# Kernel optimization log

Measured on AMD Instinct MI355X. Metric: run time of the kernel, lower is better.

The kernel has to match this reference:

```python
import jax, jax.numpy as jnp
from jax import lax
import numpy as np

B, S, V, E, H = 256, 1024, 288, 100, 128


def setup_inputs() -> dict:
    key = jax.random.key(0)
    ks = jax.random.split(key, 16)
    d = {
        "text": jax.random.randint(ks[0], (B, S), 0, V, dtype=jnp.int32),
        "emb": jax.random.normal(ks[1], (V, E), jnp.float32) * 0.1,
        "fcW": jax.random.normal(ks[2], (V, H), jnp.float32) * 0.1,
        "fcb": jax.random.normal(ks[3], (V,), jnp.float32) * 0.1,
    }
    in_dims = [E, H, H]
    for l in range(3):
        kk = jax.random.split(ks[4 + l], 4)
        d[f"Wih{l}"] = jax.random.normal(kk[0], (4 * H, in_dims[l]), jnp.float32) * 0.1
        d[f"Whh{l}"] = jax.random.normal(kk[1], (4 * H, H), jnp.float32) * 0.1
        d[f"bih{l}"] = jax.random.normal(kk[2], (4 * H,), jnp.float32) * 0.1
        d[f"bhh{l}"] = jax.random.normal(kk[3], (4 * H,), jnp.float32) * 0.1
    return d


def _lstm_layer(x, Wih, Whh, bih, bhh):
    # x: [S, B, in]; PyTorch gate order i, f, g, o
    xg = jnp.einsum('sbe,ge->sbg', x, Wih) + (bih + bhh)  # precompute input proj [S,B,4H]
    Hh = Whh.shape[1]
    WhhT = Whh.T

    def step(carry, xg_t):
        h, c = carry
        g = xg_t + h @ WhhT
        i, f, gg, o = jnp.split(g, 4, axis=-1)
        c = jax.nn.sigmoid(f) * c + jax.nn.sigmoid(i) * jnp.tanh(gg)
        h = jax.nn.sigmoid(o) * jnp.tanh(c)
        return (h, c), h

    b = x.shape[1]
    init = (jnp.zeros((b, Hh), x.dtype), jnp.zeros((b, Hh), x.dtype))
    _, hs = lax.scan(step, init, xg)
    return hs  # [S, B, H]


def reference(text, emb, Wih0, Whh0, bih0, bhh0, Wih1, Whh1, bih1, bhh1,
              Wih2, Whh2, bih2, bhh2, fcW, fcb):
    # embedding (dropout is identity in eval mode)
    x = emb[text]                  # [B, S, E]
    x = jnp.transpose(x, (1, 0, 2))  # time-major [S, B, E]
    x = _lstm_layer(x, Wih0, Whh0, bih0, bhh0)
    x = _lstm_layer(x, Wih1, Whh1, bih1, bhh1)
    x = _lstm_layer(x, Wih2, Whh2, bih2, bhh2)
    # fc head; original returns prediction.transpose(0,1) -> [S, B, V]
    pred = jnp.einsum('sbh,vh->sbv', x, fcW) + fcb
    return pred
```

## Files before the change

### kernel.cpp

```cpp
#include <hip/hip_runtime.h>
#include <cstddef>
#include <cstdint>

#define BB 256
#define SS 1024
#define VV 288
#define EE 100
#define HH 128
#define G4 512
#define CH 16
#define NCH (SS / CH)

typedef _Float16 half8 __attribute__((ext_vector_type(8)));
typedef float f32x4 __attribute__((ext_vector_type(4)));
typedef float f32x2 __attribute__((ext_vector_type(2)));

__device__ __forceinline__ f32x2 exp2_2(f32x2 a) {
    f32x2 r;
    r[0] = __builtin_amdgcn_exp2f(a[0]);
    r[1] = __builtin_amdgcn_exp2f(a[1]);
    return r;
}
__device__ __forceinline__ f32x2 rcp_2(f32x2 a) {
    f32x2 r;
    r[0] = __builtin_amdgcn_rcpf(a[0]);
    r[1] = __builtin_amdgcn_rcpf(a[1]);
    return r;
}
__device__ __forceinline__ f32x2 vmin2(f32x2 a, float m) {
    f32x2 r;
    r[0] = fminf(a[0], m);
    r[1] = fminf(a[1], m);
    return r;
}

__device__ __forceinline__ f32x2 lstm_pair(
    f32x2 gi, f32x2 gf, f32x2 gg, f32x2 go, f32x2& cc)
{
    const float L1 = -1.4426950408889634f;
    const float L2 = -2.8853900817779268f;
    const f32x2 one = {1.0f, 1.0f};
    f32x2 ai = exp2_2(gi * L1);
    f32x2 bg = exp2_2(vmin2(gg * L2, 80.0f));
    f32x2 af = exp2_2(gf * L1);
    f32x2 sf = rcp_2(af + one);
    f32x2 it = (one - bg) * rcp_2((ai + one) * (bg + one));
    cc = __builtin_elementwise_fma(sf, cc, it);
    f32x2 dc = exp2_2(vmin2(cc * L2, 80.0f));
    f32x2 ao = exp2_2(go * L1);
    return (one - dc) * rcp_2((ao + one) * (dc + one));
}

__global__ __launch_bounds__(512) void proj_kernel(
    const float* __restrict__ emb, const float* __restrict__ Wih0,
    const float* __restrict__ bih0, const float* __restrict__ bhh0,
    float* __restrict__ table)
{
    __shared__ float er[EE];
    const int v = blockIdx.x;
    const int j = threadIdx.x;
    for (int e = j; e < EE; e += 512) er[e] = emb[v * EE + e];
    __syncthreads();
    float acc = bih0[j] + bhh0[j];
    const float* wr = Wih0 + j * EE;
#pragma unroll 4
    for (int e = 0; e < EE; e++) acc = fmaf(er[e], wr[e], acc);
    table[v * G4 + j] = acc;
}

__global__ __launch_bounds__(256) void pack_fc(
    const float* __restrict__ W, _Float16* __restrict__ out)
{
    const int tid = blockIdx.x * 256 + threadIdx.x;
    const int e  = tid & 7;
    const int l  = (tid >> 3) & 63;
    const int f  = tid >> 9;
    const int kc = f & 3, nt = f >> 2;
    const int n = nt * 16 + (l & 15);
    const int k = kc * 32 + (l >> 4) * 8 + e;
    out[tid] = (_Float16)W[n * HH + k];
}

__global__ __launch_bounds__(512)
__attribute__((amdgpu_waves_per_eu(2, 2)))
void lstm_pipe(const int* __restrict__ text, const float* __restrict__ table,
               const float* Whh0f,
               const float* Wih1f, const float* Whh1f,
               const float* __restrict__ bih1, const float* __restrict__ bhh1,
               const float* Wih2f, const float* Whh2f,
               const float* __restrict__ bih2, const float* __restrict__ bhh2,
               _Float16* hX, _Float16* hY, int* prog)
{
    __shared__ int tokL[SS * 16];
    __shared__ _Float16 Hb[2][2048];
    const int tid = threadIdx.x;
    const int w = tid >> 6, l = tid & 63;
    const int layer = blockIdx.x >> 4;
    const int bt = blockIdx.x & 15;
    const int B0 = bt * 16;
    const int colD = l & 15, qd = l >> 4;
    const int gcol = w * 16 + colD;

    const float* WhhF = (layer == 0) ? Whh0f : ((layer == 1) ? Whh1f : Whh2f);
    const float* WihF = (layer == 2) ? Wih2f : Wih1f;
    const float* bihp = (layer == 2) ? bih2 : bih1;
    const float* bhhp = (layer == 2) ? bhh2 : bhh1;
    const _Float16* xin = (layer == 1) ? hX : hY;
    _Float16* hout = (layer == 1) ? hY : hX;
    int* prog_src = prog + (layer - 1) * 16 + bt;
    int* prog_my  = prog + layer * 16 + bt;

    half8 whh[4][4], wih[4][4];
#pragma unroll
    for (int gt = 0; gt < 4; gt++)
#pragma unroll
        for (int kc = 0; kc < 4; kc++) {
            const int n = gt * 128 + gcol;
            const int k0 = kc * 32 + qd * 8;
            const float4 a0 = *(const float4*)(WhhF + (size_t)n * HH + k0);
            const float4 a1 = *(const float4*)(WhhF + (size_t)n * HH + k0 + 4);
            half8 hf;
            hf[0] = (_Float16)a0.x; hf[1] = (_Float16)a0.y;
            hf[2] = (_Float16)a0.z; hf[3] = (_Float16)a0.w;
            hf[4] = (_Float16)a1.x; hf[5] = (_Float16)a1.y;
            hf[6] = (_Float16)a1.z; hf[7] = (_Float16)a1.w;
            whh[gt][kc] = hf;
            if (layer) {
                const float4 b0 = *(const float4*)(WihF + (size_t)n * HH + k0);
                const float4 b1 = *(const float4*)(WihF + (size_t)n * HH + k0 + 4);
                half8 hg;
                hg[0] = (_Float16)b0.x; hg[1] = (_Float16)b0.y;
                hg[2] = (_Float16)b0.z; hg[3] = (_Float16)b0.w;
                hg[4] = (_Float16)b1.x; hg[5] = (_Float16)b1.y;
                hg[6] = (_Float16)b1.z; hg[7] = (_Float16)b1.w;
                wih[gt][kc] = hg;
            }
        }
    f32x4 bias_frag[4];
#pragma unroll
    for (int gt = 0; gt < 4; gt++) {
        float b = 0.0f;
        if (layer) {
            const int g = gt * 128 + gcol;
            b = bihp[g] + bhhp[g];
        }
        bias_frag[gt] = (f32x4){b, b, b, b};
    }
    if (layer == 0) {
        for (int kk = 0; kk < 32; kk++) {
            const int lin = kk * 512 + tid;
            const int b = lin >> 10, t = lin & 1023;
            tokL[t * 16 + b] = text[(((size_t)B0 + b) << 10) | t];
        }
    }
    for (int i = tid; i < 2048; i += 512) Hb[0][i] = (_Float16)0.0f;
    f32x2 c_acc0 = {0.f, 0.f}, c_acc1 = {0.f, 0.f};

    int rd_idx[4], wr_idx[4];
#pragma unroll
    for (int kc = 0; kc < 4; kc++)
        rd_idx[kc] = (colD * 128 + kc * 32 + qd * 8) ^ ((colD & 7) << 3);
#pragma unroll
    for (int r = 0; r < 4; r++) {
        const int rr = 4 * qd + r;
        wr_idx[r] = (rr * 128 + gcol) ^ ((rr & 7) << 3);
    }
    _Float16* houtp = hout + ((size_t)B0 + 4 * qd) * HH + gcol;
    __syncthreads();

    auto wait_src = [&](int target) {
        int v = __hip_atomic_load(prog_src, __ATOMIC_RELAXED,
                                  __HIP_MEMORY_SCOPE_AGENT);
        while (v < target) {
            __builtin_amdgcn_s_sleep(8);
            v = __hip_atomic_load(prog_src, __ATOMIC_RELAXED,
                                  __HIP_MEMORY_SCOPE_AGENT);
        }
        v = __hip_atomic_load(prog_src, __ATOMIC_ACQUIRE,
                              __HIP_MEMORY_SCOPE_AGENT);
        asm volatile("" :: "v"(v));
    };
    auto signal = [&](int c) {
        asm volatile("s_waitcnt vmcnt(0)" ::: "memory");
        __builtin_amdgcn_s_barrier();
        if (tid == 0) {
            __threadfence();
            __hip_atomic_store(prog_my, (c + 1) * CH, __ATOMIC_RELEASE,
                               __HIP_MEMORY_SCOPE_AGENT);
        }
    };
    auto finish = [&](f32x4 (&p)[4], f32x4 (&q)[4], int nxt) {
        f32x4 acc[4];
#pragma unroll
        for (int gt = 0; gt < 4; gt++) acc[gt] = p[gt] + q[gt];
        {
            f32x2 gi = {acc[0][0], acc[0][1]};
            f32x2 gf = {acc[1][0], acc[1][1]};
            f32x2 gg = {acc[2][0], acc[2][1]};
            f32x2 go = {acc[3][0], acc[3][1]};
            f32x2 hv = lstm_pair(gi, gf, gg, go, c_acc0);
            const _Float16 h0 = (_Float16)hv[0];
            const _Float16 h1 = (_Float16)hv[1];
            Hb[nxt][wr_idx[0]] = h0;
            Hb[nxt][wr_idx[1]] = h1;
            houtp[0 * HH] = h0;
            houtp[1 * HH] = h1;
        }
        {
            f32x2 gi = {acc[0][2], acc[0][3]};
            f32x2 gf = {acc[1][2], acc[1][3]};
            f32x2 gg = {acc[2][2], acc[2][3]};
            f32x2 go = {acc[3][2], acc[3][3]};
            f32x2 hv = lstm_pair(gi, gf, gg, go, c_acc1);
            const _Float16 h2 = (_Float16)hv[0];
            const _Float16 h3 = (_Float16)hv[1];
            Hb[nxt][wr_idx[2]] = h2;
            Hb[nxt][wr_idx[3]] = h3;
            houtp[2 * HH] = h2;
            houtp[3 * HH] = h3;
        }
        houtp += BB * HH;
        asm volatile("s_waitcnt lgkmcnt(0)" ::: "memory");
        __builtin_amdgcn_s_barrier();
    };

    if (layer == 0) {
        f32x4 xgA[4], xgB[4];
        {
            const int4 tk0 = *(const int4*)&tokL[4 * qd];
            const float* g0 = table + (size_t)tk0.x * G4 + gcol;
            const float* g1 = table + (size_t)tk0.y * G4 + gcol;
            const float* g2 = table + (size_t)tk0.z * G4 + gcol;
            const float* g3 = table + (size_t)tk0.w * G4 + gcol;
#pragma unroll
            for (int gt = 0; gt < 4; gt++) {
                xgA[gt][0] = g0[gt * 128];
                xgA[gt][1] = g1[gt * 128];
                xgA[gt][2] = g2[gt * 128];
                xgA[gt][3] = g3[gt * 128];
            }
        }
        auto step0 = [&](int T, int cur, f32x4 (&xgc)[4], f32x4 (&xgn)[4]) {
            half8 a_h[4];
#pragma unroll
            for (int kc = 0; kc < 4; kc++)
                a_h[kc] = *(const half8*)&Hb[cur][rd_idx[kc]];
            const int Tn = (T + 1 < SS) ? T + 1 : T;
            const int4 tkn = *(const int4*)&tokL[Tn * 16 + 4 * qd];
            f32x4 p[4], q[4];
#pragma unroll
            for (int gt = 0; gt < 4; gt++) {
                f32x4 t = __builtin_amdgcn_mfma_f32_16x16x32_f16(
                    a_h[0], whh[gt][0], xgc[gt], 0, 0, 0);
                p[gt] = __builtin_amdgcn_mfma_f32_16x16x32_f16(
                    a_h[1], whh[gt][1], t, 0, 0, 0);
                f32x4 u = __builtin_amdgcn_mfma_f32_16x16x32_f16(
                    a_h[2], whh[gt][2], (f32x4){0.f, 0.f, 0.f, 0.f}, 0, 0, 0);
                q[gt] = __builtin_amdgcn_mfma_f32_16x16x32_f16(
                    a_h[3], whh[gt][3], u, 0, 0, 0);
            }
            {
                const float* g0 = table + (size_t)tkn.x * G4 + gcol;
                const float* g1 = table + (size_t)tkn.y * G4 + gcol;
                const float* g2 = table + (size_t)tkn.z * G4 + gcol;
                const float* g3 = table + (size_t)tkn.w * G4 + gcol;
#pragma unroll
                for (int gt = 0; gt < 4; gt++) {
                    xgn[gt][0] = g0[gt * 128];
                    xgn[gt][1] = g1[gt * 128];
                    xgn[gt][2] = g2[gt * 128];
                    xgn[gt][3] = g3[gt * 128];
                }
            }
            finish(p, q, cur ^ 1);
        };
        for (int c = 0; c < NCH; c++) {
            for (int tt = 0; tt < CH; tt += 2) {
                step0(c * CH + tt,     0, xgA, xgB);
                step0(c * CH + tt + 1, 1, xgB, xgA);
            }
            signal(c);
        }
    } else {
        wait_src(2 * CH);
        const _Float16* xbase = xin + ((size_t)B0 + colD) * HH + qd * 8;
        half8 xcur[4];
        f32x4 accXA[4], accXB[4];
#pragma unroll
        for (int kc = 0; kc < 4; kc++)
            xcur[kc] = *(const half8*)(xbase + (size_t)0 * BB * HH + kc * 32);
#pragma unroll
        for (int gt = 0; gt < 4; gt++) {
            f32x4 t = bias_frag[gt];
#pragma unroll
            for (int kc = 0; kc < 4; kc++)
                t = __builtin_amdgcn_mfma_f32_16x16x32_f16(
                    xcur[kc], wih[gt][kc], t, 0, 0, 0);
            accXA[gt] = t;
        }
#pragma unroll
        for (int kc = 0; kc < 4; kc++)
            xcur[kc] = *(const half8*)(xbase + (size_t)1 * BB * HH + kc * 32);

        auto stepK = [&](int T, int cur, f32x4 (&accXc)[4], f32x4 (&accXn)[4]) {
            half8 a_h[4];
#pragma unroll
            for (int kc = 0; kc < 4; kc++)
                a_h[kc] = *(const half8*)&Hb[cur][rd_idx[kc]];
            f32x4 p[4], q[4];
#pragma unroll
            for (int gt = 0; gt < 4; gt++) {
                f32x4 t = __builtin_amdgcn_mfma_f32_16x16x32_f16(
                    a_h[0], whh[gt][0], accXc[gt], 0, 0, 0);
                p[gt] = __builtin_amdgcn_mfma_f32_16x16x32_f16(
                    a_h[1], whh[gt][1], t, 0, 0, 0);
                f32x4 u = __builtin_amdgcn_mfma_f32_16x16x32_f16(
                    a_h[2], whh[gt][2], (f32x4){0.f, 0.f, 0.f, 0.f}, 0, 0, 0);
                q[gt] = __builtin_amdgcn_mfma_f32_16x16x32_f16(
                    a_h[3], whh[gt][3], u, 0, 0, 0);
            }
#pragma unroll
            for (int gt = 0; gt < 4; gt++) {
                f32x4 t = bias_frag[gt];
#pragma unroll
                for (int kc = 0; kc < 4; kc++)
                    t = __builtin_amdgcn_mfma_f32_16x16x32_f16(
                        xcur[kc], wih[gt][kc], t, 0, 0, 0);
                accXn[gt] = t;
            }
            {
                const size_t tf =
                    (T + 2 < SS) ? (size_t)(T + 2) : (size_t)(SS - 1);
#pragma unroll
                for (int kc = 0; kc < 4; kc++)
                    xcur[kc] = *(const half8*)(xbase + tf * BB * HH + kc * 32);
            }
            finish(p, q, cur ^ 1);
        };
        for (int c = 0; c < NCH; c++) {
            if (c) {
                const int tgt = (c + 2) * CH;
                wait_src(tgt > SS ? SS : tgt);
            }
            for (int tt = 0; tt < CH; tt += 2) {
                stepK(c * CH + tt,     0, accXA, accXB);
                stepK(c * CH + tt + 1, 1, accXB, accXA);
            }
            if (layer == 1) signal(c);
        }
    }
}

__global__ __launch_bounds__(256) void fc_mfma(
    const _Float16* __restrict__ h2, const _Float16* __restrict__ pfcW,
    const float* __restrict__ fcb, float* __restrict__ out)
{
    const int tid = threadIdx.x, wv = tid >> 6, l = tid & 63;
    const int colD = l & 15, qd = l >> 4;
    const size_t m0 = (size_t)blockIdx.x * 64 + wv * 16;
    half8 a[4];
#pragma unroll
    for (int kc = 0; kc < 4; kc++)
        a[kc] = *(const half8*)(h2 + (m0 + colD) * HH + kc * 32 + qd * 8);
    float fcb_r[18];
#pragma unroll
    for (int nt = 0; nt < 18; nt++) fcb_r[nt] = fcb[nt * 16 + colD];
#pragma unroll
    for (int nt = 0; nt < 18; nt++) {
        f32x4 acc = {0.f, 0.f, 0.f, 0.f};
#pragma unroll
        for (int kc = 0; kc < 4; kc++) {
            const half8 b = *(const half8*)(pfcW + (((nt * 4 + kc) << 6) + l) * 8);
            acc = __builtin_amdgcn_mfma_f32_16x16x32_f16(a[kc], b, acc, 0, 0, 0);
        }
#pragma unroll
        for (int r = 0; r < 4; r++)
            out[(m0 + 4 * qd + r) * VV + nt * 16 + colD] = acc[r] + fcb_r[nt];
    }
}

extern "C" void kernel_launch(void* const* d_in, const int* in_sizes, int n_in,
                              void* d_out, int out_size, void* d_ws, size_t ws_size,
                              hipStream_t stream)
{
    (void)in_sizes; (void)n_in; (void)ws_size;
    const int*   text = (const int*)  d_in[0];
    const float* emb  = (const float*)d_in[1];
    const float* fcW  = (const float*)d_in[2];
    const float* fcb  = (const float*)d_in[3];
    const float* Wih0 = (const float*)d_in[4];
    const float* Whh0 = (const float*)d_in[5];
    const float* bih0 = (const float*)d_in[6];
    const float* bhh0 = (const float*)d_in[7];
    const float* Wih1 = (const float*)d_in[8];
    const float* Whh1 = (const float*)d_in[9];
    const float* bih1 = (const float*)d_in[10];
    const float* bhh1 = (const float*)d_in[11];
    const float* Wih2 = (const float*)d_in[12];
    const float* Whh2 = (const float*)d_in[13];
    const float* bih2 = (const float*)d_in[14];
    const float* bhh2 = (const float*)d_in[15];
    float* out = (float*)d_out;

    float* table = (float*)d_ws;
    _Float16* hX = (_Float16*)((char*)d_ws + 589824);
    _Float16* hY = hX + (size_t)SS * BB * HH;
    _Float16* pfcW = (_Float16*)d_ws;
    int* prog = ((int*)d_out) + ((size_t)out_size - 64);

    hipMemsetAsync(prog, 0, 64 * sizeof(int), stream);
    proj_kernel<<<VV, 512, 0, stream>>>(emb, Wih0, bih0, bhh0, table);
    lstm_pipe<<<48, 512, 0, stream>>>(text, table, Whh0,
                                      Wih1, Whh1, bih1, bhh1,
                                      Wih2, Whh2, bih2, bhh2,
                                      hX, hY, prog);
    pack_fc<<<144, 256, 0, stream>>>(fcW, pfcW);
    fc_mfma<<<4096, 256, 0, stream>>>(hX, pfcW, fcb, out);
}
```

Baseline: 1.616 ms.

## Fuse FC head into LSTM pipeline kernel and overlap it via progress flags

Removes the separate pack_fc and fc_mfma launches and appends 2048 extra blocks to the persistent lstm_pipe grid. Each extra block packs fcW into fp16 in LDS, spin-waits on the layer-2 progress counters for its timestep, and then runs the MFMA FC head for its rows. Layer 2 now signals progress after every chunk. The goal is to hide the FC head behind the recurrent pipeline and save launch overhead. The cost is that every FC block repacks the weights redundantly, and the polling blocks take CU resources and memory bandwidth while the latency-critical LSTM blocks are running.

New measurement: 1.514 ms, median of 2. -6.3%, faster.

```diff
diff --git a/kernel.cpp b/kernel.cpp
--- a/kernel.cpp
+++ b/kernel.cpp
@@ -10,6 +10,8 @@
 #define G4 512
 #define CH 16
 #define NCH (SS / CH)
+#define NPIPE 48
+#define NFC 2048
 
 typedef _Float16 half8 __attribute__((ext_vector_type(8)));
 typedef float f32x4 __attribute__((ext_vector_type(4)));
@@ -68,19 +70,6 @@
     table[v * G4 + j] = acc;
 }
 
-__global__ __launch_bounds__(256) void pack_fc(
-    const float* __restrict__ W, _Float16* __restrict__ out)
-{
-    const int tid = blockIdx.x * 256 + threadIdx.x;
-    const int e  = tid & 7;
-    const int l  = (tid >> 3) & 63;
-    const int f  = tid >> 9;
-    const int kc = f & 3, nt = f >> 2;
-    const int n = nt * 16 + (l & 15);
-    const int k = kc * 32 + (l >> 4) * 8 + e;
-    out[tid] = (_Float16)W[n * HH + k];
-}
-
 __global__ __launch_bounds__(512)
 __attribute__((amdgpu_waves_per_eu(2, 2)))
 void lstm_pipe(const int* __restrict__ text, const float* __restrict__ table,
@@ -89,11 +78,76 @@
                const float* __restrict__ bih1, const float* __restrict__ bhh1,
                const float* Wih2f, const float* Whh2f,
                const float* __restrict__ bih2, const float* __restrict__ bhh2,
-               _Float16* hX, _Float16* hY, int* prog)
+               _Float16* hX, _Float16* hY,
+               const float* __restrict__ fcW, const float* __restrict__ fcb,
+               float* __restrict__ out, int* prog)
 {
-    __shared__ int tokL[SS * 16];
-    __shared__ _Float16 Hb[2][2048];
+    __shared__ __align__(16) char shraw[73728];
     const int tid = threadIdx.x;
+
+    if (blockIdx.x >= NPIPE) {
+        _Float16* pfc = (_Float16*)shraw;
+        const int blk = blockIdx.x - NPIPE;
+        for (int i = tid; i < 36864; i += 512) {
+            const int e = i & 7;
+            const int l = (i >> 3) & 63;
+            const int f = i >> 9;
+            const int kc = f & 3, nt = f >> 2;
+            const int n = nt * 16 + (l & 15);
+            const int k = kc * 32 + (l >> 4) * 8 + e;
+            pfc[i] = (_Float16)fcW[n * HH + k];
+        }
+        __syncthreads();
+        const int t = blk >> 1;
+        const int boff = (blk & 1) * 8;
+        if (tid == 0) {
+            for (int j = 0; j < 8; j++) {
+                for (;;) {
+                    int v = __hip_atomic_load(prog + 32 + boff + j,
+                                              __ATOMIC_RELAXED,
+                                              __HIP_MEMORY_SCOPE_AGENT);
+                    if ((unsigned)v > (unsigned)t) break;
+                    __builtin_amdgcn_s_sleep(64);
+                }
+            }
+        }
+        __syncthreads();
+        {
+            int v = __hip_atomic_load(prog + 32 + boff, __ATOMIC_ACQUIRE,
+                                      __HIP_MEMORY_SCOPE_AGENT);
+            asm volatile("" :: "v"(v));
+        }
+        const int wv = tid >> 6, l = tid & 63;
+        const int colD = l & 15, qd = l >> 4;
+        const size_t m0 = (size_t)blk * 128 + wv * 16;
+        half8 a[4];
+#pragma unroll
+        for (int kc = 0; kc < 4; kc++)
+            a[kc] = *(const half8*)(hX + (m0 + colD) * HH + kc * 32 + qd * 8);
+        float fcb_r[18];
+#pragma unroll
+        for (int nt = 0; nt < 18; nt++) fcb_r[nt] = fcb[nt * 16 + colD];
+#pragma unroll
+        for (int nt = 0; nt < 18; nt++) {
+            f32x4 acc = {0.f, 0.f, 0.f, 0.f};
+#pragma unroll
+            for (int kc = 0; kc < 4; kc++) {
+                const half8 b =
+                    *(const half8*)&pfc[(((nt * 4 + kc) << 6) + l) * 8];
+                acc = __builtin_amdgcn_mfma_f32_16x16x32_f16(a[kc], b, acc,
+                                                             0, 0, 0);
+            }
+#pragma unroll
+            for (int r = 0; r < 4; r++)
+                out[(m0 + 4 * qd + r) * VV + nt * 16 + colD] =
+                    acc[r] + fcb_r[nt];
+        }
+        return;
+    }
+
+    int* tokL = (int*)shraw;
+    typedef _Float16 HbRow[2048];
+    HbRow* Hb = (HbRow*)(shraw + 65536);
     const int w = tid >> 6, l = tid & 63;
     const int layer = blockIdx.x >> 4;
     const int bt = blockIdx.x & 15;
@@ -346,36 +400,8 @@
                 stepK(c * CH + tt,     0, accXA, accXB);
                 stepK(c * CH + tt + 1, 1, accXB, accXA);
             }
-            if (layer == 1) signal(c);
-        }
-    }
-}
-
-__global__ __launch_bounds__(256) void fc_mfma(
-    const _Float16* __restrict__ h2, const _Float16* __restrict__ pfcW,
-    const float* __restrict__ fcb, float* __restrict__ out)
-{
-    const int tid = threadIdx.x, wv = tid >> 6, l = tid & 63;
-    const int colD = l & 15, qd = l >> 4;
-    const size_t m0 = (size_t)blockIdx.x * 64 + wv * 16;
-    half8 a[4];
-#pragma unroll
-    for (int kc = 0; kc < 4; kc++)
-        a[kc] = *(const half8*)(h2 + (m0 + colD) * HH + kc * 32 + qd * 8);
-    float fcb_r[18];
-#pragma unroll
-    for (int nt = 0; nt < 18; nt++) fcb_r[nt] = fcb[nt * 16 + colD];
-#pragma unroll
-    for (int nt = 0; nt < 18; nt++) {
-        f32x4 acc = {0.f, 0.f, 0.f, 0.f};
-#pragma unroll
-        for (int kc = 0; kc < 4; kc++) {
-            const half8 b = *(const half8*)(pfcW + (((nt * 4 + kc) << 6) + l) * 8);
-            acc = __builtin_amdgcn_mfma_f32_16x16x32_f16(a[kc], b, acc, 0, 0, 0);
-        }
-#pragma unroll
-        for (int r = 0; r < 4; r++)
-            out[(m0 + 4 * qd + r) * VV + nt * 16 + colD] = acc[r] + fcb_r[nt];
+            signal(c);
+        }
     }
 }
 
@@ -405,15 +431,13 @@
     float* table = (float*)d_ws;
     _Float16* hX = (_Float16*)((char*)d_ws + 589824);
     _Float16* hY = hX + (size_t)SS * BB * HH;
-    _Float16* pfcW = (_Float16*)d_ws;
     int* prog = ((int*)d_out) + ((size_t)out_size - 64);
 
     hipMemsetAsync(prog, 0, 64 * sizeof(int), stream);
     proj_kernel<<<VV, 512, 0, stream>>>(emb, Wih0, bih0, bhh0, table);
-    lstm_pipe<<<48, 512, 0, stream>>>(text, table, Whh0,
-                                      Wih1, Whh1, bih1, bhh1,
-                                      Wih2, Whh2, bih2, bhh2,
-                                      hX, hY, prog);
-    pack_fc<<<144, 256, 0, stream>>>(fcW, pfcW);
-    fc_mfma<<<4096, 256, 0, stream>>>(hX, pfcW, fcb, out);
-}
+    lstm_pipe<<<NPIPE + NFC, 512, 0, stream>>>(
+        text, table, Whh0,
+        Wih1, Whh1, bih1, bhh1,
+        Wih2, Whh2, bih2, bhh2,
+        hX, hY, fcW, fcb, out, prog);
+}
```
